# Kernel tuning notes

Hardware: AMD Instinct MI355X
Metric: run time of the kernel (lower is better)

## Reference

```python
import jax, jax.numpy as jnp
import numpy as np

B, NP, NV, E = 256, 500, 50, 128
FP, FV = 16, 16
DEG_P, DEG_V = 6, 4


def setup_inputs() -> dict:
    key = jax.random.key(0)
    ks = jax.random.split(key, 16)
    rng = np.random.default_rng(0)

    def edges(nb, n, deg):
        per = deg * n
        off = np.repeat(np.arange(nb, dtype=np.int32) * n, per)
        ei = off[None, :] + rng.integers(0, n, size=(2, nb * per)).astype(np.int32)
        return jnp.asarray(ei)

    inp = {
        "p_x": jax.random.normal(ks[0], (B * NP, FP), jnp.float32),
        "v_x": jax.random.normal(ks[1], (B * NV, FV), jnp.float32),
        "p_edge_index": edges(B, NP, DEG_P),
        "v_edge_index": edges(B, NV, DEG_V),
        "p_batch": jnp.asarray(np.repeat(np.arange(B, dtype=np.int32), NP)),
        "v_batch": jnp.asarray(np.repeat(np.arange(B, dtype=np.int32), NV)),
    }

    def lin(k, fi, fo):
        s = 1.0 / np.sqrt(fi)
        kw, kb = jax.random.split(k)
        return (jax.random.uniform(kw, (fi, fo), jnp.float32, -s, s),
                jax.random.uniform(kb, (fo,), jnp.float32, -s, s))

    layers = [("pW0", "pb0", FP, E), ("pW1", "pb1", E, E), ("pW2", "pb2", E, E),
              ("vW0", "vb0", FV, E), ("vW1", "vb1", E, E), ("vW2", "vb2", E, E),
              ("hW1", "hb1", 4 * E, 2 * E), ("hW2", "hb2", 2 * E, E), ("hW3", "hb3", E, 1)]
    for j, (wn, bn, fi, fo) in enumerate(layers):
        W, b = lin(ks[2 + j], fi, fo)
        inp[wn] = W
        inp[bn] = b
    return inp


def _gcn(h, src, dst, dinv, W, b):
    # GCNConv: out[i] = sum_{j->i} dinv[j]*dinv[i] * (h[j] @ W) + dinv[i]^2 * (h[i] @ W) + b
    xw = h @ W
    msg = xw[src] * (dinv[src] * dinv[dst])[:, None]
    agg = jax.ops.segment_sum(msg, dst, num_segments=h.shape[0])
    return agg + xw * (dinv * dinv)[:, None] + b


def _encoder(x, edge_index, batch, W0, b0, W1, b1, W2, b2, nb, npg):
    N = x.shape[0]
    src, dst = edge_index[0], edge_index[1]
    h0 = x @ W0 + b0                                   # node_init_embeddings [N, E]
    ones_e = jnp.ones(src.shape[0], x.dtype)
    deg = 1.0 + jax.ops.segment_sum(ones_e, dst, num_segments=N)  # includes self loop
    dinv = jax.lax.rsqrt(deg)
    h = jax.nn.relu(_gcn(h0, src, dst, dinv, W1, b1))
    h = _gcn(h, src, dst, dinv, W2, b2)                # node_embeddings [N, E]
    counts = jax.ops.segment_sum(jnp.ones(N, x.dtype), batch, num_segments=nb)
    graph = jax.ops.segment_sum(h, batch, num_segments=nb) / counts[:, None]  # [nb, E]
    hd = h.reshape(nb, npg, -1)                        # to_dense_batch (equal-size graphs)
    h0d = h0.reshape(nb, npg, -1)
    gr = jnp.broadcast_to(graph[:, None, :], hd.shape)
    concat = jnp.concatenate([hd, h0d, gr], axis=-1)   # [nb, npg, 3E]
    mask = jnp.ones((nb, npg), bool)
    return graph, concat, mask


def reference(p_x, v_x, p_edge_index, v_edge_index, p_batch, v_batch,
              pW0, pb0, pW1, pb1, pW2, pb2,
              vW0, vb0, vW1, vb1, vW2, vb2,
              hW1, hb1, hW2, hb2, hW3, hb3):
    p_graph, _, _ = _encoder(p_x, p_edge_index, p_batch, pW0, pb0, pW1, pb1, pW2, pb2, B, NP)
    _, v_concat, v_mask = _encoder(v_x, v_edge_index, v_batch, vW0, vb0, vW1, vb1, vW2, vb2, B, NV)
    pg_rep = jnp.broadcast_to(p_graph[:, None, :], (B, NV, p_graph.shape[-1]))
    x = jnp.concatenate([v_concat, pg_rep], axis=-1)   # [B, NV, 4E]
    h = jax.nn.leaky_relu(x @ hW1 + hb1)
    h = jax.nn.leaky_relu(h @ hW2 + hb2)
    logits = (h @ hW3 + hb3)[..., 0]                   # [B, NV]
    return jnp.where(v_mask, logits, jnp.float32(-1e9))
```

## Files before the change

kernel.cpp:

```cpp
#include <hip/hip_runtime.h>
#include <hip/hip_bf16.h>

#define NP_TOT 128000
#define NV_TOT 12800
#define EP_EDGES 768000
#define EV_EDGES 51200
#define NB 256
#define PEPG 3000
#define VEPG 200
#define VCAP 24

typedef short bf16x8 __attribute__((ext_vector_type(8)));
typedef float f32x4 __attribute__((ext_vector_type(4)));

static __device__ __forceinline__ unsigned short f2bf(float f) {
    unsigned u = __builtin_bit_cast(unsigned, f);
    unsigned r = u + 0x7FFFu + ((u >> 16) & 1u);
    return (unsigned short)(r >> 16);
}
static __device__ __forceinline__ float bf2f(unsigned short h) {
    return __builtin_bit_cast(float, (unsigned)h << 16);
}

static __device__ __forceinline__ void frag_elem(const float* __restrict__ W,
                                                 short* __restrict__ Fh,
                                                 short* __restrict__ Fl,
                                                 int K, int M, int e) {
    if (e >= K * M) return;
    int col = e % M, kk = e / M;
    int ks = kk >> 5, rem = kk & 31, fq = rem >> 3, j = rem & 7;
    float v = W[(size_t)kk * M + col];
    unsigned short h = f2bf(v);
    size_t dst = (((size_t)col * (K >> 5) + ks) * 4 + fq) * 8 + j;
    Fh[dst] = (short)h;
    Fl[dst] = (short)f2bf(v - bf2f(h));
}

__global__ __launch_bounds__(256) void prep_k(
    const float* __restrict__ pW0, const float* __restrict__ pb0,
    const float* __restrict__ pW1,
    float* __restrict__ W01, float* __restrict__ b01,
    const float* __restrict__ vW1, short* __restrict__ W1vh, short* __restrict__ W1vl,
    const float* __restrict__ vW2, short* __restrict__ W2vh, short* __restrict__ W2vl,
    const float* __restrict__ hW1, short* __restrict__ H1h, short* __restrict__ H1l,
    const float* __restrict__ hW2, short* __restrict__ H2h, short* __restrict__ H2l) {
    int bid = blockIdx.x, t = threadIdx.x;
    if (bid == 0) {
        if (t < 128) {
            int col = t;
            float acc[17];
            #pragma unroll
            for (int r = 0; r < 17; r++) acc[r] = 0.f;
            for (int i = 0; i < 128; i++) {
                float w1 = pW1[i * 128 + col];
                #pragma unroll
                for (int r = 0; r < 16; r++) acc[r] += pW0[r * 128 + i] * w1;
                acc[16] += pb0[i] * w1;
            }
            #pragma unroll
            for (int r = 0; r < 16; r++) W01[r * 128 + col] = acc[r];
            b01[col] = acc[16];
        }
    } else if (bid < 65) {
        frag_elem(vW1, W1vh, W1vl, 128, 128, (bid - 1) * 256 + t);
    } else if (bid < 129) {
        frag_elem(vW2, W2vh, W2vl, 128, 128, (bid - 65) * 256 + t);
    } else if (bid < 641) {
        frag_elem(hW1, H1h, H1l, 512, 256, (bid - 129) * 256 + t);
    } else {
        frag_elem(hW2, H2h, H2l, 256, 128, (bid - 641) * 256 + t);
    }
}

__global__ __launch_bounds__(512) void pfused3(const float* __restrict__ x,
                                               const int* __restrict__ ei,
                                               const float* __restrict__ W01,
                                               const float* __restrict__ b01,
                                               const float* __restrict__ b1,
                                               float* __restrict__ p_gz) {
    __shared__ char lds[108544];
    float* sx = (float*)lds;
    unsigned short* sadj = (unsigned short*)(lds + 34816);
    char*  zb    = lds + 59392;
    float* sdinv = (float*)(lds + 100352);
    int*   scnt  = (int*)(lds + 102400);
    float* sbeta = (float*)(lds + 104448);
    float* scsum = (float*)(lds + 106496);

    const int t = threadIdx.x;
    const int b = blockIdx.x;

    scnt[t] = 0; scsum[t] = 0.f;
    const float4* x4 = (const float4*)(x + (size_t)b * 500 * 16);
    for (int i = t; i < 2000; i += 512) {
        float4 v = x4[i];
        int n = i >> 2, q = i & 3;
        float* dst = &sx[n * 17 + q * 4];
        dst[0] = v.x; dst[1] = v.y; dst[2] = v.z; dst[3] = v.w;
    }
    __syncthreads();

    const int* esrc = ei + (size_t)b * PEPG;
    const int* edst = ei + EP_EDGES + (size_t)b * PEPG;
    const int base = b * 500;

    for (int e = t; e < PEPG; e += 512) {
        int s = esrc[e] - base, d = edst[e] - base;
        int slot = atomicAdd(&scnt[d], 1);
        if (slot < VCAP) sadj[d * VCAP + slot] = (unsigned short)s;
    }
    __syncthreads();
    sdinv[t] = rsqrtf(1.0f + (float)scnt[t]);
    __syncthreads();

    for (int e = t; e < PEPG; e += 512)
        atomicAdd(&scsum[esrc[e] - base], sdinv[edst[e] - base]);

    {
        int cg = t & 7, nb_ = t >> 3, c0 = cg * 2;
        #pragma unroll
        for (int pass = 0; pass < 8; pass++) {
            int n = pass * 64 + nb_;
            char* zr = zb + n * 80 + cg * 4;
            if (n < 500) {
                float di = sdinv[n];
                int d = scnt[n]; if (d > VCAP) d = VCAP;
                const unsigned short* ap = sadj + n * VCAP;
                float a0 = 0.f, a1 = 0.f, ts = 0.f;
                for (int e = 0; e < d; e++) {
                    int jl = ap[e];
                    float dj = sdinv[jl];
                    a0 += dj * sx[jl * 17 + c0];
                    a1 += dj * sx[jl * 17 + c0 + 1];
                    ts += dj;
                }
                float z0 = di * (di * sx[n * 17 + c0] + a0);
                float z1 = di * (di * sx[n * 17 + c0 + 1] + a1);
                unsigned short h0 = f2bf(z0), h1 = f2bf(z1);
                unsigned short l0 = f2bf(z0 - bf2f(h0)), l1 = f2bf(z1 - bf2f(h1));
                *(unsigned*)(zr)      = (unsigned)h0 | ((unsigned)h1 << 16);
                *(unsigned*)(zr + 32) = (unsigned)l0 | ((unsigned)l1 << 16);
                if (cg == 0) sbeta[n] = di * (di + ts);
            } else {
                *(unsigned*)(zr) = 0u;
                *(unsigned*)(zr + 32) = 0u;
                if (cg == 0) sbeta[n] = 0.f;
            }
        }
    }
    __syncthreads();

    scsum[t] = (t < 500) ? sdinv[t] * (sdinv[t] + scsum[t]) * (1.0f / 500.0f) : 0.f;
    __syncthreads();

    const int lane = t & 63;
    const int wvi = t >> 6;
    const int fr = lane & 15;
    const int fq = lane >> 4;
    const int col = wvi * 16 + fr;

    bf16x8 B1, B2;
    {
        float wt[8];
        #pragma unroll
        for (int j = 0; j < 8; j++)
            wt[j] = W01[(size_t)((fq * 8 + j) & 15) * 128 + col];
        short b1a[8], b2a[8];
        #pragma unroll
        for (int j = 0; j < 8; j++) {
            int kk = fq * 8 + j;
            unsigned short h = f2bf(wt[j]);
            b1a[j] = (short)h;
            b2a[j] = (kk < 16) ? (short)f2bf(wt[j] - bf2f(h)) : (short)0;
        }
        B1 = (bf16x8){b1a[0],b1a[1],b1a[2],b1a[3],b1a[4],b1a[5],b1a[6],b1a[7]};
        B2 = (bf16x8){b2a[0],b2a[1],b2a[2],b2a[3],b2a[4],b2a[5],b2a[6],b2a[7]};
    }

    float b01c = b01[col];
    float b1c = b1[col];
    float pools = 0.f;
    #pragma unroll
    for (int ch = 0; ch < 4; ch++) {
        f32x4 acc[8];
        #pragma unroll
        for (int m = 0; m < 8; m++) acc[m] = (f32x4){0.f, 0.f, 0.f, 0.f};
        #pragma unroll
        for (int m = 0; m < 8; m++) {
            int r = ch * 128 + m * 16 + fr;
            bf16x8 a = *(bf16x8*)(zb + r * 80 + fq * 16);
            acc[m] = __builtin_amdgcn_mfma_f32_16x16x32_bf16(a, B1, acc[m], 0, 0, 0);
            acc[m] = __builtin_amdgcn_mfma_f32_16x16x32_bf16(a, B2, acc[m], 0, 0, 0);
        }
        #pragma unroll
        for (int m = 0; m < 8; m++)
            #pragma unroll
            for (int j = 0; j < 4; j++) {
                int rl = ch * 128 + m * 16 + fq * 4 + j;
                float v = fmaxf(acc[m][j] + sbeta[rl] * b01c + b1c, 0.f);
                pools += scsum[rl] * v;
            }
    }
    pools += __shfl_xor(pools, 16);
    pools += __shfl_xor(pools, 32);
    if (fq == 0) p_gz[(size_t)b * 128 + col] = pools;
}

#define LB 0
#define LC 34816
#define LD 67584
#define LE 100352
#define E_SDINV (LE)
#define E_SCNT  (LE + 256)
#define E_SADJ  (LE + 512)
#define E_SVG   (LE + 5376)
#define E_VGH   (LE + 5888)
#define E_VGL   (LE + 6144)
#define E_PGH   (LE + 6400)
#define E_PGL   (LE + 6656)
#define E_WSUM  (LE + 6912)
__global__ __launch_bounds__(512) void vhead_k(
    const float* __restrict__ v_x,
    const int* __restrict__ v_ei,
    const float* __restrict__ W0, const float* __restrict__ b0,
    const short* __restrict__ W1h, const short* __restrict__ W1l,
    const float* __restrict__ b1,
    const short* __restrict__ W2h, const short* __restrict__ W2l,
    const float* __restrict__ b2,
    const float* __restrict__ p_gz,
    const float* __restrict__ pW2, const float* __restrict__ pb2,
    const short* __restrict__ H1h, const short* __restrict__ H1l,
    const float* __restrict__ hb1,
    const short* __restrict__ H2h, const short* __restrict__ H2l,
    const float* __restrict__ hb2,
    const float* __restrict__ w3, const float* __restrict__ b3,
    float* __restrict__ out) {
    __shared__ char lds[109312];
    const int t = threadIdx.x;
    const int b = blockIdx.x;
    const int lane = t & 63;
    const int wv = t >> 6;
    const int fr = lane & 15;
    const int fq = lane >> 4;
    float* Bf = (float*)(lds + LB);
    float* sdinv = (float*)(lds + E_SDINV);
    int*   scnt  = (int*)(lds + E_SCNT);
    int*   sadj  = (int*)(lds + E_SADJ);

    if (t < 64) scnt[t] = 0;
    *(float4*)(lds + LC + t * 16) = *((const float4*)W0 + t);
    {
        int col = t & 127, q = t >> 7;
        const float* gz = p_gz + (size_t)b * 128;
        float s = 0.f;
        #pragma unroll
        for (int k = 0; k < 32; k++)
            s += gz[q * 32 + k] * pW2[(size_t)(q * 32 + k) * 128 + col];
        ((float*)(lds + E_WSUM))[q * 128 + col] = s;
    }
    __syncthreads();

    if (t < VEPG) {
        int s = v_ei[b * VEPG + t] - b * 50;
        int d = v_ei[EV_EDGES + b * VEPG + t] - b * 50;
        int slot = atomicAdd(&scnt[d], 1);
        if (slot < VCAP) sadj[d * VCAP + slot] = s;
    }
    __syncthreads();

    if (t < 64)
        sdinv[t] = (t < 50) ? rsqrtf(1.0f + (float)scnt[t]) : 0.f;
    if (t < 128) {
        float* part = (float*)(lds + E_WSUM);
        float v = part[t] + part[128 + t] + part[256 + t] + part[384 + t] + pb2[t];
        unsigned short h = f2bf(v);
        ((short*)(lds + E_PGH))[t] = (short)h;
        ((short*)(lds + E_PGL))[t] = (short)f2bf(v - bf2f(h));
    }
    {
        int n = t >> 3, cg = t & 7;
        if (n < 50) {
            const float* sW0 = (const float*)(lds + LC);
            const float4* xr = (const float4*)(v_x + (size_t)(b * 50 + n) * 16);
            float4 x0 = xr[0], x1 = xr[1], x2 = xr[2], x3 = xr[3];
            float xv[16] = {x0.x,x0.y,x0.z,x0.w, x1.x,x1.y,x1.z,x1.w,
                            x2.x,x2.y,x2.z,x2.w, x3.x,x3.y,x3.z,x3.w};
            #pragma unroll
            for (int cc = 0; cc < 16; cc++) {
                int c = cg * 16 + cc;
                float a = b0[c];
                #pragma unroll
                for (int k = 0; k < 16; k++) a += xv[k] * sW0[k * 128 + c];
                Bf[n * 136 + c] = a;
            }
        }
    }
    __syncthreads();

    {
        int r = t >> 3, f0 = (t & 7) * 16;
        #pragma unroll
        for (int w8 = 0; w8 < 8; w8++) {
            int f = f0 + 2 * w8;
            float v0 = Bf[r * 136 + f], v1 = Bf[r * 136 + f + 1];
            unsigned short h0 = f2bf(v0), h1 = f2bf(v1);
            unsigned short l0 = f2bf(v0 - bf2f(h0)), l1 = f2bf(v1 - bf2f(h1));
            int q = (256 + 2 * f) ^ ((r & 7) << 4);
            *(unsigned*)(lds + LC + r * 512 + q) = (unsigned)h0 | ((unsigned)h1 << 16);
            *(unsigned*)(lds + LD + r * 512 + q) = (unsigned)l0 | ((unsigned)l1 << 16);
        }
        int n = r;
        if (n < 50) {
            float di = sdinv[n];
            int d = scnt[n]; if (d > VCAP) d = VCAP;
            float acc[16];
            #pragma unroll
            for (int cc = 0; cc < 16; cc++) acc[cc] = di * Bf[n * 136 + f0 + cc];
            const int* ap = sadj + n * VCAP;
            #pragma unroll
            for (int e = 0; e < 12; e++) {
                bool valid = e < d;
                int jl = valid ? ap[e] : n;
                float dj = valid ? sdinv[jl] : 0.f;
                #pragma unroll
                for (int cc = 0; cc < 16; cc++) acc[cc] += dj * Bf[jl * 136 + f0 + cc];
            }
            for (int e = 12; e < d; e++) {
                int jl = ap[e];
                float dj = sdinv[jl];
                #pragma unroll
                for (int cc = 0; cc < 16; cc++) acc[cc] += dj * Bf[jl * 136 + f0 + cc];
            }
            #pragma unroll
            for (int w8 = 0; w8 < 8; w8++) {
                float z0 = di * acc[2 * w8], z1 = di * acc[2 * w8 + 1];
                unsigned short h0 = f2bf(z0), h1 = f2bf(z1);
                unsigned short l0 = f2bf(z0 - bf2f(h0)), l1 = f2bf(z1 - bf2f(h1));
                int q = (2 * (f0 + 2 * w8)) ^ ((n & 7) << 4);
                *(unsigned*)(lds + LC + n * 512 + q) = (unsigned)h0 | ((unsigned)h1 << 16);
                *(unsigned*)(lds + LD + n * 512 + q) = (unsigned)l0 | ((unsigned)l1 << 16);
            }
        }
    }
    __syncthreads();

    {
        const int col = wv * 16 + fr;
        bf16x8 bh[4], bl[4];
        #pragma unroll
        for (int ks = 0; ks < 4; ks++) {
            int base = ((col * 4 + ks) * 4 + fq) * 8;
            bh[ks] = *(const bf16x8*)&W1h[base];
            bl[ks] = *(const bf16x8*)&W1l[base];
        }
        f32x4 acc[4];
        #pragma unroll
        for (int m = 0; m < 4; m++) acc[m] = (f32x4){0.f,0.f,0.f,0.f};
        #pragma unroll
        for (int ks = 0; ks < 4; ks++) {
            int kb = ks * 64 + fq * 16;
            #pragma unroll
            for (int m = 0; m < 4; m++) {
                int r = m * 16 + fr;
                int off = r * 512 + (kb ^ ((r & 7) << 4));
                bf16x8 ah = *(bf16x8*)(lds + LC + off);
                bf16x8 al = *(bf16x8*)(lds + LD + off);
                acc[m] = __builtin_amdgcn_mfma_f32_16x16x32_bf16(ah, bh[ks], acc[m], 0, 0, 0);
                acc[m] = __builtin_amdgcn_mfma_f32_16x16x32_bf16(ah, bl[ks], acc[m], 0, 0, 0);
                acc[m] = __builtin_amdgcn_mfma_f32_16x16x32_bf16(al, bh[ks], acc[m], 0, 0, 0);
            }
        }
        float b1c = b1[col];
        #pragma unroll
        for (int m = 0; m < 4; m++)
            #pragma unroll
            for (int j = 0; j < 4; j++) {
                int row = m * 16 + fq * 4 + j;
                Bf[row * 136 + col] = fmaxf(acc[m][j] + b1c, 0.f);
            }
    }
    __syncthreads();

    {
        int n = t >> 3, f0 = (t & 7) * 16;
        if (n < 50) {
            float di = sdinv[n];
            int d = scnt[n]; if (d > VCAP) d = VCAP;
            float acc[16];
            #pragma unroll
            for (int cc = 0; cc < 16; cc++) acc[cc] = di * Bf[n * 136 + f0 + cc];
            const int* ap = sadj + n * VCAP;
            #pragma unroll
            for (int e = 0; e < 12; e++) {
                bool valid = e < d;
                int jl = valid ? ap[e] : n;
                float dj = valid ? sdinv[jl] : 0.f;
                #pragma unroll
                for (int cc = 0; cc < 16; cc++) acc[cc] += dj * Bf[jl * 136 + f0 + cc];
            }
            for (int e = 12; e < d; e++) {
                int jl = ap[e];
                float dj = sdinv[jl];
                #pragma unroll
                for (int cc = 0; cc < 16; cc++) acc[cc] += dj * Bf[jl * 136 + f0 + cc];
            }
            #pragma unroll
            for (int w8 = 0; w8 < 8; w8++) {
                float z0 = di * acc[2 * w8], z1 = di * acc[2 * w8 + 1];
                unsigned short h0 = f2bf(z0), h1 = f2bf(z1);
                unsigned short l0 = f2bf(z0 - bf2f(h0)), l1 = f2bf(z1 - bf2f(h1));
                int q = (2 * (f0 + 2 * w8)) ^ ((n & 7) << 4);
                *(unsigned*)(lds + LC + n * 512 + q) = (unsigned)h0 | ((unsigned)h1 << 16);
                *(unsigned*)(lds + LD + n * 512 + q) = (unsigned)l0 | ((unsigned)l1 << 16);
            }
        }
    }
    __syncthreads();

    float h2v[4][4];
    {
        const int col = wv * 16 + fr;
        bf16x8 bh[4], bl[4];
        #pragma unroll
        for (int ks = 0; ks < 4; ks++) {
            int base = ((col * 4 + ks) * 4 + fq) * 8;
            bh[ks] = *(const bf16x8*)&W2h[base];
            bl[ks] = *(const bf16x8*)&W2l[base];
        }
        f32x4 acc[4];
        #pragma unroll
        for (int m = 0; m < 4; m++) acc[m] = (f32x4){0.f,0.f,0.f,0.f};
        #pragma unroll
        for (int ks = 0; ks < 4; ks++) {
            int kb = ks * 64 + fq * 16;
            #pragma unroll
            for (int m = 0; m < 4; m++) {
                int r = m * 16 + fr;
                int off = r * 512 + (kb ^ ((r & 7) << 4));
                bf16x8 ah = *(bf16x8*)(lds + LC + off);
                bf16x8 al = *(bf16x8*)(lds + LD + off);
                acc[m] = __builtin_amdgcn_mfma_f32_16x16x32_bf16(ah, bh[ks], acc[m], 0, 0, 0);
                acc[m] = __builtin_amdgcn_mfma_f32_16x16x32_bf16(ah, bl[ks], acc[m], 0, 0, 0);
                acc[m] = __builtin_amdgcn_mfma_f32_16x16x32_bf16(al, bh[ks], acc[m], 0, 0, 0);
            }
        }
        float b2c = b2[col];
        #pragma unroll
        for (int m = 0; m < 4; m++)
            #pragma unroll
            for (int j = 0; j < 4; j++) h2v[m][j] = acc[m][j] + b2c;
    }
    __syncthreads();

    {
        const int col = wv * 16 + fr;
        float s = 0.f;
        #pragma unroll
        for (int m = 0; m < 4; m++)
            #pragma unroll
            for (int j = 0; j < 4; j++) {
                int row = m * 16 + fq * 4 + j;
                float v = h2v[m][j];
                unsigned short h = f2bf(v);
                unsigned short l = f2bf(v - bf2f(h));
                int q = (2 * col) ^ ((row & 7) << 4);
                *(short*)(lds + LC + row * 512 + q) = (short)h;
                *(short*)(lds + LD + row * 512 + q) = (short)l;
                if (row < 50) s += v;
            }
        s += __shfl_xor(s, 16); s += __shfl_xor(s, 32);
        if (fq == 0) ((float*)(lds + E_SVG))[col] = s * (1.0f / 50.0f);
    }
    __syncthreads();

    if (t < 128) {
        float v = ((float*)(lds + E_SVG))[t];
        unsigned short h = f2bf(v);
        ((short*)(lds + E_VGH))[t] = (short)h;
        ((short*)(lds + E_VGL))[t] = (short)f2bf(v - bf2f(h));
    }
    __syncthreads();

    f32x4 accT[4][2];
    #pragma unroll
    for (int m = 0; m < 4; m++)
        #pragma unroll
        for (int nf = 0; nf < 2; nf++) accT[m][nf] = (f32x4){0.f,0.f,0.f,0.f};
    {
        #pragma unroll
        for (int ks = 0; ks < 16; ks++) {
            bf16x8 bh[2], bl[2];
            #pragma unroll
            for (int nf = 0; nf < 2; nf++) {
                int col2 = wv * 32 + nf * 16 + fr;
                int base = ((col2 * 16 + ks) * 4 + fq) * 8;
                bh[nf] = *(const bf16x8*)&H1h[base];
                bl[nf] = *(const bf16x8*)&H1l[base];
            }
            if (ks < 8) {
                int kb = ks * 64 + fq * 16;
                #pragma unroll
                for (int m = 0; m < 4; m++) {
                    int r = m * 16 + fr;
                    int off = r * 512 + (kb ^ ((r & 7) << 4));
                    bf16x8 ah = *(bf16x8*)(lds + LC + off);
                    bf16x8 al = *(bf16x8*)(lds + LD + off);
                    #pragma unroll
                    for (int nf = 0; nf < 2; nf++) {
                        accT[m][nf] = __builtin_amdgcn_mfma_f32_16x16x32_bf16(ah, bh[nf], accT[m][nf], 0, 0, 0);
                        accT[m][nf] = __builtin_amdgcn_mfma_f32_16x16x32_bf16(ah, bl[nf], accT[m][nf], 0, 0, 0);
                        accT[m][nf] = __builtin_amdgcn_mfma_f32_16x16x32_bf16(al, bh[nf], accT[m][nf], 0, 0, 0);
                    }
                }
            } else {
                int boff = (ks < 12) ? (E_VGH + (ks - 8) * 64 + fq * 16)
                                     : (E_PGH + (ks - 12) * 64 + fq * 16);
                int loff = boff + 256;
                bf16x8 ah = *(bf16x8*)(lds + boff);
                bf16x8 al = *(bf16x8*)(lds + loff);
                #pragma unroll
                for (int m = 0; m < 4; m++)
                    #pragma unroll
                    for (int nf = 0; nf < 2; nf++) {
                        accT[m][nf] = __builtin_amdgcn_mfma_f32_16x16x32_bf16(ah, bh[nf], accT[m][nf], 0, 0, 0);
                        accT[m][nf] = __builtin_amdgcn_mfma_f32_16x16x32_bf16(ah, bl[nf], accT[m][nf], 0, 0, 0);
                        accT[m][nf] = __builtin_amdgcn_mfma_f32_16x16x32_bf16(al, bh[nf], accT[m][nf], 0, 0, 0);
                    }
            }
        }
    }
    __syncthreads();
    {
        #pragma unroll
        for (int nf = 0; nf < 2; nf++) {
            int col2 = wv * 32 + nf * 16 + fr;
            float hc = hb1[col2];
            #pragma unroll
            for (int m = 0; m < 4; m++)
                #pragma unroll
                for (int j = 0; j < 4; j++) {
                    int row = m * 16 + fq * 4 + j;
                    float v = accT[m][nf][j] + hc;
                    v = v > 0.f ? v : 0.01f * v;
                    unsigned short h = f2bf(v);
                    unsigned short l = f2bf(v - bf2f(h));
                    int q = (2 * col2) ^ ((row & 7) << 4);
                    *(short*)(lds + LC + row * 512 + q) = (short)h;
                    *(short*)(lds + LD + row * 512 + q) = (short)l;
                }
        }
    }
    __syncthreads();

    {
        const int col3 = wv * 16 + fr;
        f32x4 acc[4];
        #pragma unroll
        for (int m = 0; m < 4; m++) acc[m] = (f32x4){0.f,0.f,0.f,0.f};
        #pragma unroll
        for (int ks = 0; ks < 8; ks++) {
            int base = ((col3 * 8 + ks) * 4 + fq) * 8;
            bf16x8 bh = *(const bf16x8*)&H2h[base];
            bf16x8 bl = *(const bf16x8*)&H2l[base];
            int kb = ks * 64 + fq * 16;
            #pragma unroll
            for (int m = 0; m < 4; m++) {
                int r = m * 16 + fr;
                int off = r * 512 + (kb ^ ((r & 7) << 4));
                bf16x8 ah = *(bf16x8*)(lds + LC + off);
                bf16x8 al = *(bf16x8*)(lds + LD + off);
                acc[m] = __builtin_amdgcn_mfma_f32_16x16x32_bf16(ah, bh, acc[m], 0, 0, 0);
                acc[m] = __builtin_amdgcn_mfma_f32_16x16x32_bf16(ah, bl, acc[m], 0, 0, 0);
                acc[m] = __builtin_amdgcn_mfma_f32_16x16x32_bf16(al, bh, acc[m], 0, 0, 0);
            }
        }
        float hc = hb2[col3], wc = w3[col3];
        float p[4][4];
        #pragma unroll
        for (int m = 0; m < 4; m++)
            #pragma unroll
            for (int j = 0; j < 4; j++) {
                float v = acc[m][j] + hc;
                v = v > 0.f ? v : 0.01f * v;
                p[m][j] = v * wc;
            }
        #pragma unroll
        for (int m = 0; m < 4; m++)
            #pragma unroll
            for (int j = 0; j < 4; j++) {
                p[m][j] += __shfl_xor(p[m][j], 1);
                p[m][j] += __shfl_xor(p[m][j], 2);
                p[m][j] += __shfl_xor(p[m][j], 4);
                p[m][j] += __shfl_xor(p[m][j], 8);
            }
        if (fr == 0) {
            float* wsum = (float*)(lds + E_WSUM);
            #pragma unroll
            for (int m = 0; m < 4; m++)
                #pragma unroll
                for (int j = 0; j < 4; j++)
                    wsum[wv * 64 + m * 16 + fq * 4 + j] = p[m][j];
        }
    }
    __syncthreads();
    if (t < 50) {
        float* wsum = (float*)(lds + E_WSUM);
        float s = 0.f;
        #pragma unroll
        for (int w8 = 0; w8 < 8; w8++) s += wsum[w8 * 64 + t];
        out[b * 50 + t] = s + b3[0];
    }
}

extern "C" void kernel_launch(void* const* d_in, const int* in_sizes, int n_in,
                              void* d_out, int out_size, void* d_ws, size_t ws_size,
                              hipStream_t stream) {
    const float* p_x = (const float*)d_in[0];
    const float* v_x = (const float*)d_in[1];
    const int* p_ei = (const int*)d_in[2];
    const int* v_ei = (const int*)d_in[3];
    const float* pW0 = (const float*)d_in[6];  const float* pb0 = (const float*)d_in[7];
    const float* pW1 = (const float*)d_in[8];  const float* pb1 = (const float*)d_in[9];
    const float* pW2 = (const float*)d_in[10]; const float* pb2 = (const float*)d_in[11];
    const float* vW0 = (const float*)d_in[12]; const float* vb0 = (const float*)d_in[13];
    const float* vW1 = (const float*)d_in[14]; const float* vb1 = (const float*)d_in[15];
    const float* vW2 = (const float*)d_in[16]; const float* vb2 = (const float*)d_in[17];
    const float* hW1 = (const float*)d_in[18]; const float* hb1 = (const float*)d_in[19];
    const float* hW2 = (const float*)d_in[20]; const float* hb2 = (const float*)d_in[21];
    const float* hW3 = (const float*)d_in[22]; const float* hb3 = (const float*)d_in[23];

    char* w = (char*)d_ws;
    size_t off = 0;
    auto alloc = [&](size_t bytes) { char* p = w + off; off += (bytes + 255) & ~size_t(255); return p; };
    float* p_gz = (float*)alloc((size_t)NB * 128 * 4);
    float* W01  = (float*)alloc((size_t)16 * 128 * 4);
    float* b01  = (float*)alloc((size_t)128 * 4);
    short* W1vh = (short*)alloc((size_t)128 * 128 * 2);
    short* W1vl = (short*)alloc((size_t)128 * 128 * 2);
    short* W2vh = (short*)alloc((size_t)128 * 128 * 2);
    short* W2vl = (short*)alloc((size_t)128 * 128 * 2);
    short* H1h  = (short*)alloc((size_t)512 * 256 * 2);
    short* H1l  = (short*)alloc((size_t)512 * 256 * 2);
    short* H2h  = (short*)alloc((size_t)256 * 128 * 2);
    short* H2l  = (short*)alloc((size_t)256 * 128 * 2);

    prep_k<<<769, 256, 0, stream>>>(pW0, pb0, pW1, W01, b01,
                                    vW1, W1vh, W1vl, vW2, W2vh, W2vl,
                                    hW1, H1h, H1l, hW2, H2h, H2l);
    pfused3<<<NB, 512, 0, stream>>>(p_x, p_ei, W01, b01, pb1, p_gz);
    vhead_k<<<NB, 512, 0, stream>>>(v_x, v_ei,
                                    vW0, vb0, W1vh, W1vl, vb1, W2vh, W2vl, vb2,
                                    p_gz, pW2, pb2, H1h, H1l, hb1, H2h, H2l, hb2,
                                    hW3, hb3, (float*)d_out);
}
```

Measured before the change: 79.20 us.

## Chunk pfused3 aggregation into the MFMA loop to shrink LDS; pad vhead pitch

pfused3 now builds the bf16 hi/lo aggregated features 128 nodes at a time, inside the MFMA loop, instead of for all 500 nodes up front. This shrinks the z buffer and cuts LDS from about 106KB to 76KB, which could let two 512-thread blocks share a CU. The cost is extra barriers per chunk. In vhead_k the fp32 feature pitch changes from 136 to 137 and the init embedding column mapping is interleaved, both to reduce LDS bank conflicts; the later LDS regions are shifted to fit.

```diff
diff --git a/kernel.cpp b/kernel.cpp
--- a/kernel.cpp
+++ b/kernel.cpp
@@ -9,6 +9,7 @@
 #define PEPG 3000
 #define VEPG 200
 #define VCAP 24
+#define PITCHV 137
 
 typedef short bf16x8 __attribute__((ext_vector_type(8)));
 typedef float f32x4 __attribute__((ext_vector_type(4)));
@@ -78,14 +79,14 @@
                                                const float* __restrict__ b01,
                                                const float* __restrict__ b1,
                                                float* __restrict__ p_gz) {
-    __shared__ char lds[108544];
+    __shared__ char lds[77824];
     float* sx = (float*)lds;
     unsigned short* sadj = (unsigned short*)(lds + 34816);
     char*  zb    = lds + 59392;
-    float* sdinv = (float*)(lds + 100352);
-    int*   scnt  = (int*)(lds + 102400);
-    float* sbeta = (float*)(lds + 104448);
-    float* scsum = (float*)(lds + 106496);
+    float* sdinv = (float*)(lds + 69632);
+    int*   scnt  = (int*)(lds + 71680);
+    float* sbeta = (float*)(lds + 73728);
+    float* scsum = (float*)(lds + 75776);
 
     const int t = threadIdx.x;
     const int b = blockIdx.x;
@@ -115,13 +116,43 @@
 
     for (int e = t; e < PEPG; e += 512)
         atomicAdd(&scsum[esrc[e] - base], sdinv[edst[e] - base]);
-
-    {
-        int cg = t & 7, nb_ = t >> 3, c0 = cg * 2;
-        #pragma unroll
-        for (int pass = 0; pass < 8; pass++) {
-            int n = pass * 64 + nb_;
-            char* zr = zb + n * 80 + cg * 4;
+    __syncthreads();
+    scsum[t] = (t < 500) ? sdinv[t] * (sdinv[t] + scsum[t]) * (1.0f / 500.0f) : 0.f;
+
+    const int lane = t & 63;
+    const int wvi = t >> 6;
+    const int fr = lane & 15;
+    const int fq = lane >> 4;
+    const int col = wvi * 16 + fr;
+    bf16x8 B1, B2;
+    {
+        float wt[8];
+        #pragma unroll
+        for (int j = 0; j < 8; j++)
+            wt[j] = W01[(size_t)((fq * 8 + j) & 15) * 128 + col];
+        short b1a[8], b2a[8];
+        #pragma unroll
+        for (int j = 0; j < 8; j++) {
+            int kk = fq * 8 + j;
+            unsigned short h = f2bf(wt[j]);
+            b1a[j] = (short)h;
+            b2a[j] = (kk < 16) ? (short)f2bf(wt[j] - bf2f(h)) : (short)0;
+        }
+        B1 = (bf16x8){b1a[0],b1a[1],b1a[2],b1a[3],b1a[4],b1a[5],b1a[6],b1a[7]};
+        B2 = (bf16x8){b2a[0],b2a[1],b2a[2],b2a[3],b2a[4],b2a[5],b2a[6],b2a[7]};
+    }
+    float b01c = b01[col];
+    float b1c = b1[col];
+    float pools = 0.f;
+
+    const int cg = t & 7, nb_ = t >> 3, c0 = cg * 2;
+    #pragma unroll
+    for (int ch = 0; ch < 4; ch++) {
+        __syncthreads();
+        #pragma unroll
+        for (int pass = 0; pass < 2; pass++) {
+            int n = ch * 128 + pass * 64 + nb_;
+            char* zr = zb + (pass * 64 + nb_) * 80 + cg * 4;
             if (n < 500) {
                 float di = sdinv[n];
                 int d = scnt[n]; if (d > VCAP) d = VCAP;
@@ -147,48 +178,14 @@
                 if (cg == 0) sbeta[n] = 0.f;
             }
         }
-    }
-    __syncthreads();
-
-    scsum[t] = (t < 500) ? sdinv[t] * (sdinv[t] + scsum[t]) * (1.0f / 500.0f) : 0.f;
-    __syncthreads();
-
-    const int lane = t & 63;
-    const int wvi = t >> 6;
-    const int fr = lane & 15;
-    const int fq = lane >> 4;
-    const int col = wvi * 16 + fr;
-
-    bf16x8 B1, B2;
-    {
-        float wt[8];
-        #pragma unroll
-        for (int j = 0; j < 8; j++)
-            wt[j] = W01[(size_t)((fq * 8 + j) & 15) * 128 + col];
-        short b1a[8], b2a[8];
-        #pragma unroll
-        for (int j = 0; j < 8; j++) {
-            int kk = fq * 8 + j;
-            unsigned short h = f2bf(wt[j]);
-            b1a[j] = (short)h;
-            b2a[j] = (kk < 16) ? (short)f2bf(wt[j] - bf2f(h)) : (short)0;
-        }
-        B1 = (bf16x8){b1a[0],b1a[1],b1a[2],b1a[3],b1a[4],b1a[5],b1a[6],b1a[7]};
-        B2 = (bf16x8){b2a[0],b2a[1],b2a[2],b2a[3],b2a[4],b2a[5],b2a[6],b2a[7]};
-    }
-
-    float b01c = b01[col];
-    float b1c = b1[col];
-    float pools = 0.f;
-    #pragma unroll
-    for (int ch = 0; ch < 4; ch++) {
+        __syncthreads();
         f32x4 acc[8];
         #pragma unroll
         for (int m = 0; m < 8; m++) acc[m] = (f32x4){0.f, 0.f, 0.f, 0.f};
         #pragma unroll
         for (int m = 0; m < 8; m++) {
-            int r = ch * 128 + m * 16 + fr;
-            bf16x8 a = *(bf16x8*)(zb + r * 80 + fq * 16);
+            int rl = m * 16 + fr;
+            bf16x8 a = *(bf16x8*)(zb + rl * 80 + fq * 16);
             acc[m] = __builtin_amdgcn_mfma_f32_16x16x32_bf16(a, B1, acc[m], 0, 0, 0);
             acc[m] = __builtin_amdgcn_mfma_f32_16x16x32_bf16(a, B2, acc[m], 0, 0, 0);
         }
@@ -207,9 +204,9 @@
 }
 
 #define LB 0
-#define LC 34816
-#define LD 67584
-#define LE 100352
+#define LC 35072
+#define LD 67840
+#define LE 100608
 #define E_SDINV (LE)
 #define E_SCNT  (LE + 256)
 #define E_SADJ  (LE + 512)
@@ -235,7 +232,7 @@
     const float* __restrict__ hb2,
     const float* __restrict__ w3, const float* __restrict__ b3,
     float* __restrict__ out) {
-    __shared__ char lds[109312];
+    __shared__ char lds[109568];
     const int t = threadIdx.x;
     const int b = blockIdx.x;
     const int lane = t & 63;
@@ -287,11 +284,11 @@
                             x2.x,x2.y,x2.z,x2.w, x3.x,x3.y,x3.z,x3.w};
             #pragma unroll
             for (int cc = 0; cc < 16; cc++) {
-                int c = cg * 16 + cc;
+                int c = cg + cc * 8;
                 float a = b0[c];
                 #pragma unroll
                 for (int k = 0; k < 16; k++) a += xv[k] * sW0[k * 128 + c];
-                Bf[n * 136 + c] = a;
+                Bf[n * PITCHV + c] = a;
             }
         }
     }
@@ -302,7 +299,7 @@
         #pragma unroll
         for (int w8 = 0; w8 < 8; w8++) {
             int f = f0 + 2 * w8;
-            float v0 = Bf[r * 136 + f], v1 = Bf[r * 136 + f + 1];
+            float v0 = Bf[r * PITCHV + f], v1 = Bf[r * PITCHV + f + 1];
             unsigned short h0 = f2bf(v0), h1 = f2bf(v1);
             unsigned short l0 = f2bf(v0 - bf2f(h0)), l1 = f2bf(v1 - bf2f(h1));
             int q = (256 + 2 * f) ^ ((r & 7) << 4);
@@ -315,7 +312,7 @@
             int d = scnt[n]; if (d > VCAP) d = VCAP;
             float acc[16];
             #pragma unroll
-            for (int cc = 0; cc < 16; cc++) acc[cc] = di * Bf[n * 136 + f0 + cc];
+            for (int cc = 0; cc < 16; cc++) acc[cc] = di * Bf[n * PITCHV + f0 + cc];
             const int* ap = sadj + n * VCAP;
             #pragma unroll
             for (int e = 0; e < 12; e++) {
@@ -323,13 +320,13 @@
                 int jl = valid ? ap[e] : n;
                 float dj = valid ? sdinv[jl] : 0.f;
                 #pragma unroll
-                for (int cc = 0; cc < 16; cc++) acc[cc] += dj * Bf[jl * 136 + f0 + cc];
+                for (int cc = 0; cc < 16; cc++) acc[cc] += dj * Bf[jl * PITCHV + f0 + cc];
             }
             for (int e = 12; e < d; e++) {
                 int jl = ap[e];
                 float dj = sdinv[jl];
                 #pragma unroll
-                for (int cc = 0; cc < 16; cc++) acc[cc] += dj * Bf[jl * 136 + f0 + cc];
+                for (int cc = 0; cc < 16; cc++) acc[cc] += dj * Bf[jl * PITCHV + f0 + cc];
             }
             #pragma unroll
             for (int w8 = 0; w8 < 8; w8++) {
@@ -376,7 +373,7 @@
             #pragma unroll
             for (int j = 0; j < 4; j++) {
                 int row = m * 16 + fq * 4 + j;
-                Bf[row * 136 + col] = fmaxf(acc[m][j] + b1c, 0.f);
+                Bf[row * PITCHV + col] = fmaxf(acc[m][j] + b1c, 0.f);
             }
     }
     __syncthreads();
@@ -388,7 +385,7 @@
             int d = scnt[n]; if (d > VCAP) d = VCAP;
             float acc[16];
             #pragma unroll
-            for (int cc = 0; cc < 16; cc++) acc[cc] = di * Bf[n * 136 + f0 + cc];
+            for (int cc = 0; cc < 16; cc++) acc[cc] = di * Bf[n * PITCHV + f0 + cc];
             const int* ap = sadj + n * VCAP;
             #pragma unroll
             for (int e = 0; e < 12; e++) {
@@ -396,13 +393,13 @@
                 int jl = valid ? ap[e] : n;
                 float dj = valid ? sdinv[jl] : 0.f;
                 #pragma unroll
-                for (int cc = 0; cc < 16; cc++) acc[cc] += dj * Bf[jl * 136 + f0 + cc];
+                for (int cc = 0; cc < 16; cc++) acc[cc] += dj * Bf[jl * PITCHV + f0 + cc];
             }
             for (int e = 12; e < d; e++) {
                 int jl = ap[e];
                 float dj = sdinv[jl];
                 #pragma unroll
-                for (int cc = 0; cc < 16; cc++) acc[cc] += dj * Bf[jl * 136 + f0 + cc];
+                for (int cc = 0; cc < 16; cc++) acc[cc] += dj * Bf[jl * PITCHV + f0 + cc];
             }
             #pragma unroll
             for (int w8 = 0; w8 < 8; w8++) {
```

Measured after the change: 86.30 us. +9.0%, slower.
